# Kernel optimization log

Hardware: AMD Instinct MI355X
Metric: run time of the kernel (lower is better)

## Reference

```python
import jax, jax.numpy as jnp
import numpy as np

N = 500000      # examples = M * (nr+1)
K = 20          # context set size (indices[:, 3:])
NR = 24         # negatives per positive
H = 128         # hidden_channels == node feature dim
NODES = 10000   # ingredient vocabulary


def setup_inputs() -> dict:
    key = jax.random.key(0)
    ks = jax.random.split(key, 6)
    indices = jax.random.randint(ks[0], (N, 3 + K), 0, NODES)
    x = jax.random.normal(ks[1], (NODES, H), dtype=jnp.float32)
    scale = 0.02
    W1 = jax.random.normal(ks[2], (H, 3 * H), dtype=jnp.float32) * scale
    b1 = jnp.zeros((H,), jnp.float32)
    W2 = jax.random.normal(ks[3], (H // 2, H), dtype=jnp.float32) * scale
    b2 = jnp.zeros((H // 2,), jnp.float32)
    W3 = jax.random.normal(ks[4], (1, H // 2), dtype=jnp.float32) * scale
    b3 = jnp.zeros((1,), jnp.float32)
    return {"indices": indices, "nr": NR, "x": x,
            "W1": W1, "b1": b1, "W2": W2, "b2": b2, "W3": W3, "b3": b3}


def _embed_context(ctx_idx, x, nr):
    # ctx_idx: [N, K]; one context row per group of (nr+1) examples
    new_idx = ctx_idx[:-1:nr + 1]                 # [M, K]
    emb = x[new_idx]                               # [M, K, H] gather
    s = emb.sum(axis=1)                            # [M, H]
    norm = jnp.maximum((new_idx > 0).sum(axis=1), 1).astype(x.dtype)[:, None]
    mean = s / norm                                # masked mean over context
    return jnp.repeat(mean, nr + 1, axis=0)        # broadcast back to [N, H]


def reference(indices, nr, x, W1, b1, W2, b2, W3, b3):
    ing1 = x[indices[:, 0]]                        # [N, H]
    ing2 = x[indices[:, 1]]                        # [N, H]
    set_emb = _embed_context(indices[:, 3:], x, nr)  # [N, H]
    y = jnp.concatenate([ing1, ing2, set_emb], axis=1)  # [N, 3H]
    y = jax.nn.relu(y @ W1.T + b1)
    y = jax.nn.relu(y @ W2.T + b2)
    return y @ W3.T + b3                           # [N, 1]
```

## Files before the change

### kernel.cpp

```cpp
#include <hip/hip_runtime.h>
#include <hip/hip_bf16.h>

#define N_ROWS   500000
#define NR1      25
#define NGROUPS  20000
#define KCTX     20
#define H        128
#define NODES    10000
#define IDX_COLS 23

typedef __attribute__((ext_vector_type(8))) short short8;
typedef __attribute__((ext_vector_type(4))) float f32x4;

__device__ __forceinline__ unsigned pkbf(float lo, float hi) {
  __hip_bfloat162 h = __float22bfloat162_rn(make_float2(lo, hi));
  union { __hip_bfloat162 h; unsigned u; } c; c.h = h;
  return c.u;
}
__device__ __forceinline__ float bf2f(unsigned short u) {
  union { unsigned u; float f; } c; c.u = ((unsigned)u) << 16; return c.f;
}

__global__ __launch_bounds__(256) void k_pack(
    const int* __restrict__ indices, int2* __restrict__ idx2) {
  const int r = blockIdx.x * 256 + threadIdx.x;
  if (r < N_ROWS) {
    idx2[r] = make_int2(indices[(size_t)r * IDX_COLS + 0],
                        indices[(size_t)r * IDX_COLS + 1]);
  }
}

__global__ __launch_bounds__(256) void k_precompute(
    const float* __restrict__ x, const float* __restrict__ W1,
    unsigned short* __restrict__ Pb) {
  __shared__ short w_hi[128][132];
  __shared__ short w_lo[128][132];

  const int tid   = threadIdx.x;
  const int m     = blockIdx.y;
  const int tbase = blockIdx.x * 128;

  for (int it = 0; it < 16; ++it) {
    const int f  = it * 256 + tid;
    const int j  = f >> 5;
    const int q4 = f & 31;
    const float4 v = *(const float4*)(W1 + (size_t)j * (3 * H) + m * H + q4 * 4);
    const unsigned h01 = pkbf(v.x, v.y);
    const unsigned h23 = pkbf(v.z, v.w);
    union { unsigned u; unsigned short s[2]; } a, b;
    a.u = h01; b.u = h23;
    const unsigned l01 = pkbf(v.x - bf2f(a.s[0]), v.y - bf2f(a.s[1]));
    const unsigned l23 = pkbf(v.z - bf2f(b.s[0]), v.w - bf2f(b.s[1]));
    *(unsigned*)&w_hi[j][q4 * 4]     = h01;
    *(unsigned*)&w_hi[j][q4 * 4 + 2] = h23;
    *(unsigned*)&w_lo[j][q4 * 4]     = l01;
    *(unsigned*)&w_lo[j][q4 * 4 + 2] = l23;
  }
  __syncthreads();

  const int lane = tid & 63;
  const int wv   = tid >> 6;
  const int col  = lane & 15;
  const int quad = lane >> 4;
  const int nwb  = tbase + wv * 32;

  f32x4 acc[2][8];
#pragma unroll
  for (int rt = 0; rt < 2; ++rt)
#pragma unroll
    for (int ct = 0; ct < 8; ++ct) acc[rt][ct] = (f32x4)(0.f);

#pragma unroll
  for (int kt = 0; kt < 4; ++kt) {
    short8 Ah[2], Al[2];
#pragma unroll
    for (int rt = 0; rt < 2; ++rt) {
      int node = nwb + rt * 16 + col;
      if (node > NODES - 1) node = NODES - 1;
      const float4* xr = (const float4*)(x + (size_t)node * H);
      const int f4 = kt * 8 + quad * 2;
      const float4 v0 = xr[f4], v1 = xr[f4 + 1];
      union { short8 v; unsigned u[4]; unsigned short s[8]; } Hh, Ll;
      Hh.u[0] = pkbf(v0.x, v0.y);
      Hh.u[1] = pkbf(v0.z, v0.w);
      Hh.u[2] = pkbf(v1.x, v1.y);
      Hh.u[3] = pkbf(v1.z, v1.w);
      Ll.u[0] = pkbf(v0.x - bf2f(Hh.s[0]), v0.y - bf2f(Hh.s[1]));
      Ll.u[1] = pkbf(v0.z - bf2f(Hh.s[2]), v0.w - bf2f(Hh.s[3]));
      Ll.u[2] = pkbf(v1.x - bf2f(Hh.s[4]), v1.y - bf2f(Hh.s[5]));
      Ll.u[3] = pkbf(v1.z - bf2f(Hh.s[6]), v1.w - bf2f(Hh.s[7]));
      Ah[rt] = Hh.v; Al[rt] = Ll.v;
    }
#pragma unroll
    for (int ct = 0; ct < 8; ++ct) {
      const short8 Bh = *(const short8*)&w_hi[ct * 16 + col][kt * 32 + quad * 8];
      const short8 Bl = *(const short8*)&w_lo[ct * 16 + col][kt * 32 + quad * 8];
#pragma unroll
      for (int rt = 0; rt < 2; ++rt) {
        acc[rt][ct] = __builtin_amdgcn_mfma_f32_16x16x32_bf16(Ah[rt], Bh, acc[rt][ct], 0, 0, 0);
        acc[rt][ct] = __builtin_amdgcn_mfma_f32_16x16x32_bf16(Al[rt], Bh, acc[rt][ct], 0, 0, 0);
        acc[rt][ct] = __builtin_amdgcn_mfma_f32_16x16x32_bf16(Ah[rt], Bl, acc[rt][ct], 0, 0, 0);
      }
    }
  }

  unsigned short* __restrict__ Pm = Pb + (size_t)m * NODES * H;
#pragma unroll
  for (int rt = 0; rt < 2; ++rt) {
#pragma unroll
    for (int reg = 0; reg < 4; ++reg) {
      const int node = nwb + rt * 16 + quad * 4 + reg;
      if (node < NODES) {
#pragma unroll
        for (int ct = 0; ct < 8; ++ct) {
          union { unsigned u; unsigned short s[2]; } c;
          c.u = pkbf(acc[rt][ct][reg], 0.f);
          Pm[(size_t)node * H + ct * 16 + col] = c.s[0];
        }
      }
    }
  }
}

__global__ __launch_bounds__(256) void k_main(
    const int* __restrict__ indices, const int2* __restrict__ idx2,
    const unsigned short* __restrict__ P1b, const unsigned short* __restrict__ P2b,
    const unsigned short* __restrict__ P3b,
    const float* __restrict__ W2, const float* __restrict__ b1,
    const float* __restrict__ b2, const float* __restrict__ W3,
    const float* __restrict__ b3, float* __restrict__ out) {
  __shared__ short w2s[64][136];
  __shared__ float cgs[7][132];

  const int tid   = threadIdx.x;
  const int rbase = blockIdx.x * 128;

  for (int idx = tid; idx < 64 * 64; idx += 256) {
    const int n  = idx >> 6;
    const int kp = idx & 63;
    const float2 w = *(const float2*)(W2 + (size_t)n * H + kp * 2);
    *(unsigned*)&w2s[n][kp * 2] = pkbf(w.x, w.y);
  }

  const int gbase = rbase / NR1;
  {
    int rlast = rbase + 127; if (rlast > N_ROWS - 1) rlast = N_ROWS - 1;
    const int G   = rlast / NR1 - gbase + 1;
    const int j   = tid & 127;
    const int sub = tid >> 7;
#pragma unroll
    for (int it = 0; it < 4; ++it) {
      const int gi = it * 2 + sub;
      if (gi < G) {
        const int* __restrict__ rowidx =
            indices + (size_t)(gbase + gi) * NR1 * IDX_COLS + 3;
        float s = 0.f; int cnt = 0;
#pragma unroll
        for (int c = 0; c < KCTX; ++c) {
          const int idx = rowidx[c];
          s += bf2f(P3b[(size_t)idx * H + j]);
          cnt += (idx > 0) ? 1 : 0;
        }
        const float norm = (float)((cnt > 1) ? cnt : 1);
        cgs[gi][j] = b1[j] + s / norm;
      }
    }
  }
  __syncthreads();

  const int lane = tid & 63;
  const int wv   = tid >> 6;
  const int col  = lane & 15;
  const int quad = lane >> 4;
  const int Rw   = rbase + wv * 32;

  int gl[2];
  const short8* pa[2];
  const short8* pb[2];
#pragma unroll
  for (int rt = 0; rt < 2; ++rt) {
    const int r  = Rw + rt * 16 + col;
    const int rc = (r < N_ROWS) ? r : (N_ROWS - 1);
    const int2 ii = idx2[rc];
    pa[rt] = (const short8*)(P1b + (size_t)ii.x * H);
    pb[rt] = (const short8*)(P2b + (size_t)ii.y * H);
    gl[rt] = rc / NR1 - gbase;
  }

  short8 A[2][4];
#pragma unroll
  for (int rt = 0; rt < 2; ++rt) {
#pragma unroll
    for (int kt = 0; kt < 4; ++kt) {
      union { short8 v; unsigned short s[8]; } ua, ub;
      ua.v = pa[rt][kt * 4 + quad];
      ub.v = pb[rt][kt * 4 + quad];
      const float4 c0 = *(const float4*)&cgs[gl[rt]][kt * 32 + quad * 8];
      const float4 c1 = *(const float4*)&cgs[gl[rt]][kt * 32 + quad * 8 + 4];
      const float h0 = fmaxf(bf2f(ua.s[0]) + bf2f(ub.s[0]) + c0.x, 0.f);
      const float h1 = fmaxf(bf2f(ua.s[1]) + bf2f(ub.s[1]) + c0.y, 0.f);
      const float h2 = fmaxf(bf2f(ua.s[2]) + bf2f(ub.s[2]) + c0.z, 0.f);
      const float h3 = fmaxf(bf2f(ua.s[3]) + bf2f(ub.s[3]) + c0.w, 0.f);
      const float h4 = fmaxf(bf2f(ua.s[4]) + bf2f(ub.s[4]) + c1.x, 0.f);
      const float h5 = fmaxf(bf2f(ua.s[5]) + bf2f(ub.s[5]) + c1.y, 0.f);
      const float h6 = fmaxf(bf2f(ua.s[6]) + bf2f(ub.s[6]) + c1.z, 0.f);
      const float h7 = fmaxf(bf2f(ua.s[7]) + bf2f(ub.s[7]) + c1.w, 0.f);
      union { short8 v; unsigned u[4]; } pk;
      pk.u[0] = pkbf(h0, h1);
      pk.u[1] = pkbf(h2, h3);
      pk.u[2] = pkbf(h4, h5);
      pk.u[3] = pkbf(h6, h7);
      A[rt][kt] = pk.v;
    }
  }

  f32x4 acc[2][4];
#pragma unroll
  for (int rt = 0; rt < 2; ++rt)
#pragma unroll
    for (int ct = 0; ct < 4; ++ct) acc[rt][ct] = (f32x4)(0.f);

#pragma unroll
  for (int kt = 0; kt < 4; ++kt) {
#pragma unroll
    for (int ct = 0; ct < 4; ++ct) {
      const short8 Bf = *(const short8*)&w2s[ct * 16 + col][kt * 32 + quad * 8];
#pragma unroll
      for (int rt = 0; rt < 2; ++rt)
        acc[rt][ct] = __builtin_amdgcn_mfma_f32_16x16x32_bf16(
            A[rt][kt], Bf, acc[rt][ct], 0, 0, 0);
    }
  }

  float b2v[4], w3v[4];
#pragma unroll
  for (int ct = 0; ct < 4; ++ct) {
    b2v[ct] = b2[ct * 16 + col];
    w3v[ct] = W3[ct * 16 + col];
  }
  const float bias3 = b3[0];
#pragma unroll
  for (int rt = 0; rt < 2; ++rt) {
#pragma unroll
    for (int reg = 0; reg < 4; ++reg) {
      float s = 0.f;
#pragma unroll
      for (int ct = 0; ct < 4; ++ct)
        s += fmaxf(acc[rt][ct][reg] + b2v[ct], 0.f) * w3v[ct];
      s += __shfl_xor(s, 1);
      s += __shfl_xor(s, 2);
      s += __shfl_xor(s, 4);
      s += __shfl_xor(s, 8);
      if (col == 0) {
        const int row = Rw + rt * 16 + quad * 4 + reg;
        if (row < N_ROWS) out[row] = s + bias3;
      }
    }
  }
}

extern "C" void kernel_launch(void* const* d_in, const int* in_sizes, int n_in,
                              void* d_out, int out_size, void* d_ws, size_t ws_size,
                              hipStream_t stream) {
  const int*   indices = (const int*)  d_in[0];
  const float* x  = (const float*)d_in[2];
  const float* W1 = (const float*)d_in[3];
  const float* b1 = (const float*)d_in[4];
  const float* W2 = (const float*)d_in[5];
  const float* b2 = (const float*)d_in[6];
  const float* W3 = (const float*)d_in[7];
  const float* b3 = (const float*)d_in[8];
  float* out = (float*)d_out;

  unsigned short* Pb  = (unsigned short*)d_ws;
  unsigned short* P1b = Pb;
  unsigned short* P2b = Pb + (size_t)NODES * H;
  unsigned short* P3b = Pb + (size_t)2 * NODES * H;
  int2* idx2 = (int2*)((char*)d_ws + (size_t)3 * NODES * H * sizeof(unsigned short));

  k_pack<<<(N_ROWS + 255) / 256, 256, 0, stream>>>(indices, idx2);
  dim3 gpre((NODES + 127) / 128, 3);
  k_precompute<<<gpre, 256, 0, stream>>>(x, W1, Pb);
  k_main<<<(N_ROWS + 127) / 128, 256, 0, stream>>>(indices, idx2, P1b, P2b, P3b,
                                                   W2, b1, b2, W3, b3, out);
}
```

Measured before the change: 169.0 us.

## Drop index pack kernel, single-pass bf16 precompute, hoist gathers before context reduction

Removes the k_pack launch and has k_main read the two ingredient indices directly from the strided index array. Issues the P1/P2 row gathers before the context-mean reduction so their latency overlaps it. Simplifies the precompute to a single bf16 MFMA pass instead of the hi/lo three-pass split, and halves the nodes per block. W2 is converted to bf16 once in the precompute kernel and read from global memory in k_main instead of being staged per block in LDS. This lowers precision of the precomputed projections and adds register pressure from the held gather data.

Result: slower. 243.1 us (+43.9%).

```diff
diff --git a/kernel.cpp b/kernel.cpp
--- a/kernel.cpp
+++ b/kernel.cpp
@@ -21,40 +21,33 @@
   union { unsigned u; float f; } c; c.u = ((unsigned)u) << 16; return c.f;
 }
 
-__global__ __launch_bounds__(256) void k_pack(
-    const int* __restrict__ indices, int2* __restrict__ idx2) {
-  const int r = blockIdx.x * 256 + threadIdx.x;
-  if (r < N_ROWS) {
-    idx2[r] = make_int2(indices[(size_t)r * IDX_COLS + 0],
-                        indices[(size_t)r * IDX_COLS + 1]);
-  }
-}
-
+#define PN 64
 __global__ __launch_bounds__(256) void k_precompute(
     const float* __restrict__ x, const float* __restrict__ W1,
-    unsigned short* __restrict__ Pb) {
-  __shared__ short w_hi[128][132];
-  __shared__ short w_lo[128][132];
+    const float* __restrict__ W2,
+    unsigned short* __restrict__ Pb, unsigned short* __restrict__ w2b) {
+  __shared__ short wlds[128][136];
 
   const int tid   = threadIdx.x;
   const int m     = blockIdx.y;
-  const int tbase = blockIdx.x * 128;
-
+  const int tbase = blockIdx.x * PN;
+
+#pragma unroll
   for (int it = 0; it < 16; ++it) {
     const int f  = it * 256 + tid;
     const int j  = f >> 5;
     const int q4 = f & 31;
     const float4 v = *(const float4*)(W1 + (size_t)j * (3 * H) + m * H + q4 * 4);
-    const unsigned h01 = pkbf(v.x, v.y);
-    const unsigned h23 = pkbf(v.z, v.w);
-    union { unsigned u; unsigned short s[2]; } a, b;
-    a.u = h01; b.u = h23;
-    const unsigned l01 = pkbf(v.x - bf2f(a.s[0]), v.y - bf2f(a.s[1]));
-    const unsigned l23 = pkbf(v.z - bf2f(b.s[0]), v.w - bf2f(b.s[1]));
-    *(unsigned*)&w_hi[j][q4 * 4]     = h01;
-    *(unsigned*)&w_hi[j][q4 * 4 + 2] = h23;
-    *(unsigned*)&w_lo[j][q4 * 4]     = l01;
-    *(unsigned*)&w_lo[j][q4 * 4 + 2] = l23;
+    *(unsigned*)&wlds[j][q4 * 4]     = pkbf(v.x, v.y);
+    *(unsigned*)&wlds[j][q4 * 4 + 2] = pkbf(v.z, v.w);
+  }
+  if (m == 2 && blockIdx.x == 0) {
+    for (int i = tid; i < 64 * 64; i += 256) {
+      const int n  = i >> 6;
+      const int kp = i & 63;
+      const float2 w = *(const float2*)(W2 + (size_t)n * H + kp * 2);
+      *(unsigned*)&w2b[(size_t)n * H + kp * 2] = pkbf(w.x, w.y);
+    }
   }
   __syncthreads();
 
@@ -62,87 +55,89 @@
   const int wv   = tid >> 6;
   const int col  = lane & 15;
   const int quad = lane >> 4;
-  const int nwb  = tbase + wv * 32;
-
-  f32x4 acc[2][8];
-#pragma unroll
-  for (int rt = 0; rt < 2; ++rt)
-#pragma unroll
-    for (int ct = 0; ct < 8; ++ct) acc[rt][ct] = (f32x4)(0.f);
-
+
+  int node = tbase + wv * 16 + col;
+  if (node > NODES - 1) node = NODES - 1;
+  const float4* __restrict__ xr = (const float4*)(x + (size_t)node * H);
+
+  short8 Af[4];
 #pragma unroll
   for (int kt = 0; kt < 4; ++kt) {
-    short8 Ah[2], Al[2];
-#pragma unroll
-    for (int rt = 0; rt < 2; ++rt) {
-      int node = nwb + rt * 16 + col;
-      if (node > NODES - 1) node = NODES - 1;
-      const float4* xr = (const float4*)(x + (size_t)node * H);
-      const int f4 = kt * 8 + quad * 2;
-      const float4 v0 = xr[f4], v1 = xr[f4 + 1];
-      union { short8 v; unsigned u[4]; unsigned short s[8]; } Hh, Ll;
-      Hh.u[0] = pkbf(v0.x, v0.y);
-      Hh.u[1] = pkbf(v0.z, v0.w);
-      Hh.u[2] = pkbf(v1.x, v1.y);
-      Hh.u[3] = pkbf(v1.z, v1.w);
-      Ll.u[0] = pkbf(v0.x - bf2f(Hh.s[0]), v0.y - bf2f(Hh.s[1]));
-      Ll.u[1] = pkbf(v0.z - bf2f(Hh.s[2]), v0.w - bf2f(Hh.s[3]));
-      Ll.u[2] = pkbf(v1.x - bf2f(Hh.s[4]), v1.y - bf2f(Hh.s[5]));
-      Ll.u[3] = pkbf(v1.z - bf2f(Hh.s[6]), v1.w - bf2f(Hh.s[7]));
-      Ah[rt] = Hh.v; Al[rt] = Ll.v;
-    }
+    const int f4 = kt * 8 + quad * 2;
+    const float4 v0 = xr[f4], v1 = xr[f4 + 1];
+    union { short8 v; unsigned u[4]; } pk;
+    pk.u[0] = pkbf(v0.x, v0.y);
+    pk.u[1] = pkbf(v0.z, v0.w);
+    pk.u[2] = pkbf(v1.x, v1.y);
+    pk.u[3] = pkbf(v1.z, v1.w);
+    Af[kt] = pk.v;
+  }
+
+  f32x4 acc[8];
+#pragma unroll
+  for (int ct = 0; ct < 8; ++ct) acc[ct] = (f32x4)(0.f);
+
+#pragma unroll
+  for (int kt = 0; kt < 4; ++kt) {
 #pragma unroll
     for (int ct = 0; ct < 8; ++ct) {
-      const short8 Bh = *(const short8*)&w_hi[ct * 16 + col][kt * 32 + quad * 8];
-      const short8 Bl = *(const short8*)&w_lo[ct * 16 + col][kt * 32 + quad * 8];
-#pragma unroll
-      for (int rt = 0; rt < 2; ++rt) {
-        acc[rt][ct] = __builtin_amdgcn_mfma_f32_16x16x32_bf16(Ah[rt], Bh, acc[rt][ct], 0, 0, 0);
-        acc[rt][ct] = __builtin_amdgcn_mfma_f32_16x16x32_bf16(Al[rt], Bh, acc[rt][ct], 0, 0, 0);
-        acc[rt][ct] = __builtin_amdgcn_mfma_f32_16x16x32_bf16(Ah[rt], Bl, acc[rt][ct], 0, 0, 0);
+      const short8 Bf = *(const short8*)&wlds[ct * 16 + col][kt * 32 + quad * 8];
+      acc[ct] = __builtin_amdgcn_mfma_f32_16x16x32_bf16(Af[kt], Bf, acc[ct], 0, 0, 0);
+    }
+  }
+
+  unsigned short* __restrict__ Pm = Pb + (size_t)m * NODES * H;
+#pragma unroll
+  for (int reg = 0; reg < 4; ++reg) {
+    const int n = tbase + wv * 16 + quad * 4 + reg;
+    if (n < NODES) {
+#pragma unroll
+      for (int ct = 0; ct < 8; ++ct) {
+        union { unsigned u; unsigned short s[2]; } c;
+        c.u = pkbf(acc[ct][reg], 0.f);
+        Pm[(size_t)n * H + ct * 16 + col] = c.s[0];
       }
     }
   }
-
-  unsigned short* __restrict__ Pm = Pb + (size_t)m * NODES * H;
-#pragma unroll
-  for (int rt = 0; rt < 2; ++rt) {
-#pragma unroll
-    for (int reg = 0; reg < 4; ++reg) {
-      const int node = nwb + rt * 16 + quad * 4 + reg;
-      if (node < NODES) {
-#pragma unroll
-        for (int ct = 0; ct < 8; ++ct) {
-          union { unsigned u; unsigned short s[2]; } c;
-          c.u = pkbf(acc[rt][ct][reg], 0.f);
-          Pm[(size_t)node * H + ct * 16 + col] = c.s[0];
-        }
-      }
-    }
-  }
 }
 
 __global__ __launch_bounds__(256) void k_main(
-    const int* __restrict__ indices, const int2* __restrict__ idx2,
+    const int* __restrict__ indices,
     const unsigned short* __restrict__ P1b, const unsigned short* __restrict__ P2b,
-    const unsigned short* __restrict__ P3b,
-    const float* __restrict__ W2, const float* __restrict__ b1,
-    const float* __restrict__ b2, const float* __restrict__ W3,
-    const float* __restrict__ b3, float* __restrict__ out) {
-  __shared__ short w2s[64][136];
+    const unsigned short* __restrict__ P3b, const unsigned short* __restrict__ w2b,
+    const float* __restrict__ b1, const float* __restrict__ b2,
+    const float* __restrict__ W3, const float* __restrict__ b3,
+    float* __restrict__ out) {
   __shared__ float cgs[7][132];
 
   const int tid   = threadIdx.x;
   const int rbase = blockIdx.x * 128;
-
-  for (int idx = tid; idx < 64 * 64; idx += 256) {
-    const int n  = idx >> 6;
-    const int kp = idx & 63;
-    const float2 w = *(const float2*)(W2 + (size_t)n * H + kp * 2);
-    *(unsigned*)&w2s[n][kp * 2] = pkbf(w.x, w.y);
-  }
-
   const int gbase = rbase / NR1;
+
+  const int lane = tid & 63;
+  const int wv   = tid >> 6;
+  const int col  = lane & 15;
+  const int quad = lane >> 4;
+  const int Rw   = rbase + wv * 32;
+
+  int gl[2];
+  short8 ua[2][4], ub[2][4];
+#pragma unroll
+  for (int rt = 0; rt < 2; ++rt) {
+    const int r  = Rw + rt * 16 + col;
+    const int rc = (r < N_ROWS) ? r : (N_ROWS - 1);
+    const int i0 = indices[(size_t)rc * IDX_COLS + 0];
+    const int i1 = indices[(size_t)rc * IDX_COLS + 1];
+    const short8* __restrict__ pa = (const short8*)(P1b + (size_t)i0 * H);
+    const short8* __restrict__ pb = (const short8*)(P2b + (size_t)i1 * H);
+#pragma unroll
+    for (int kt = 0; kt < 4; ++kt) {
+      ua[rt][kt] = pa[kt * 4 + quad];
+      ub[rt][kt] = pb[kt * 4 + quad];
+    }
+    gl[rt] = rc / NR1 - gbase;
+  }
+
   {
     int rlast = rbase + 127; if (rlast > N_ROWS - 1) rlast = N_ROWS - 1;
     const int G   = rlast / NR1 - gbase + 1;
@@ -168,43 +163,24 @@
   }
   __syncthreads();
 
-  const int lane = tid & 63;
-  const int wv   = tid >> 6;
-  const int col  = lane & 15;
-  const int quad = lane >> 4;
-  const int Rw   = rbase + wv * 32;
-
-  int gl[2];
-  const short8* pa[2];
-  const short8* pb[2];
+  short8 A[2][4];
 #pragma unroll
   for (int rt = 0; rt < 2; ++rt) {
-    const int r  = Rw + rt * 16 + col;
-    const int rc = (r < N_ROWS) ? r : (N_ROWS - 1);
-    const int2 ii = idx2[rc];
-    pa[rt] = (const short8*)(P1b + (size_t)ii.x * H);
-    pb[rt] = (const short8*)(P2b + (size_t)ii.y * H);
-    gl[rt] = rc / NR1 - gbase;
-  }
-
-  short8 A[2][4];
-#pragma unroll
-  for (int rt = 0; rt < 2; ++rt) {
 #pragma unroll
     for (int kt = 0; kt < 4; ++kt) {
-      union { short8 v; unsigned short s[8]; } ua, ub;
-      ua.v = pa[rt][kt * 4 + quad];
-      ub.v = pb[rt][kt * 4 + quad];
+      union { short8 v; unsigned short s[8]; } va, vb;
+      va.v = ua[rt][kt];
+      vb.v = ub[rt][kt];
       const float4 c0 = *(const float4*)&cgs[gl[rt]][kt * 32 + quad * 8];
       const float4 c1 = *(const float4*)&cgs[gl[rt]][kt * 32 + quad * 8 + 4];
-      const float h0 = fmaxf(bf2f(ua.s[0]) + bf2f(ub.s[0]) + c0.x, 0.f);
-      const float h1 = fmaxf(bf2f(ua.s[1]) + bf2f(ub.s[1]) + c0.y, 0.f);
-      const float h2 = fmaxf(bf2f(ua.s[2]) + bf2f(ub.s[2]) + c0.z, 0.f);
-      const float h3 = fmaxf(bf2f(ua.s[3]) + bf2f(ub.s[3]) + c0.w, 0.f);
-      const float h4 = fmaxf(bf2f(ua.s[4]) + bf2f(ub.s[4]) + c1.x, 0.f);
-      const float h5 = fmaxf(bf2f(ua.s[5]) + bf2f(ub.s[5]) + c1.y, 0.f);
-      const float h6 = fmaxf(bf2f(ua.s[6]) + bf2f(ub.s[6]) + c1.z, 0.f);
-      const float h7 = fmaxf(bf2f(ua.s[7]) + bf2f(ub.s[7]) + c1.w, 0.f);
+      const float h0 = fmaxf(bf2f(va.s[0]) + bf2f(vb.s[0]) + c0.x, 0.f);
+      const float h1 = fmaxf(bf2f(va.s[1]) + bf2f(vb.s[1]) + c0.y, 0.f);
+      const float h2 = fmaxf(bf2f(va.s[2]) + bf2f(vb.s[2]) + c0.z, 0.f);
+      const float h3 = fmaxf(bf2f(va.s[3]) + bf2f(vb.s[3]) + c0.w, 0.f);
+      const float h4 = fmaxf(bf2f(va.s[4]) + bf2f(vb.s[4]) + c1.x, 0.f);
+      const float h5 = fmaxf(bf2f(va.s[5]) + bf2f(vb.s[5]) + c1.y, 0.f);
+      const float h6 = fmaxf(bf2f(va.s[6]) + bf2f(vb.s[6]) + c1.z, 0.f);
+      const float h7 = fmaxf(bf2f(va.s[7]) + bf2f(vb.s[7]) + c1.w, 0.f);
       union { short8 v; unsigned u[4]; } pk;
       pk.u[0] = pkbf(h0, h1);
       pk.u[1] = pkbf(h2, h3);
@@ -224,7 +200,8 @@
   for (int kt = 0; kt < 4; ++kt) {
 #pragma unroll
     for (int ct = 0; ct < 4; ++ct) {
-      const short8 Bf = *(const short8*)&w2s[ct * 16 + col][kt * 32 + quad * 8];
+      const short8 Bf = *(const short8*)(w2b + (size_t)(ct * 16 + col) * H +
+                                         kt * 32 + quad * 8);
 #pragma unroll
       for (int rt = 0; rt < 2; ++rt)
         acc[rt][ct] = __builtin_amdgcn_mfma_f32_16x16x32_bf16(
@@ -276,11 +253,10 @@
   unsigned short* P1b = Pb;
   unsigned short* P2b = Pb + (size_t)NODES * H;
   unsigned short* P3b = Pb + (size_t)2 * NODES * H;
-  int2* idx2 = (int2*)((char*)d_ws + (size_t)3 * NODES * H * sizeof(unsigned short));
-
-  k_pack<<<(N_ROWS + 255) / 256, 256, 0, stream>>>(indices, idx2);
-  dim3 gpre((NODES + 127) / 128, 3);
-  k_precompute<<<gpre, 256, 0, stream>>>(x, W1, Pb);
-  k_main<<<(N_ROWS + 127) / 128, 256, 0, stream>>>(indices, idx2, P1b, P2b, P3b,
-                                                   W2, b1, b2, W3, b3, out);
-}
+  unsigned short* w2b = Pb + (size_t)3 * NODES * H;
+
+  dim3 gpre((NODES + PN - 1) / PN, 3);
+  k_precompute<<<gpre, 256, 0, stream>>>(x, W1, W2, Pb, w2b);
+  k_main<<<(N_ROWS + 127) / 128, 256, 0, stream>>>(indices, P1b, P2b, P3b, w2b,
+                                                   b1, b2, W3, b3, out);
+}
```
